# Optimization experiments

Measured on AMD Instinct MI355X. Metric: run time of the kernel, lower is better.

The kernel has to match this reference:

```python
import jax, jax.numpy as jnp
import numpy as np

N = 100000
E = 1600000
IN, HID, OUT, HEADS = 256, 16, 64, 8
NEG_SLOPE = 0.2


def gat_conv(x, src, dst, W, att_s, att_d, bias, heads, out_c, concat):
    n = x.shape[0]
    h = (x @ W).reshape(n, heads, out_c)              # [N,H,C]
    a_s = jnp.einsum('nhc,hc->nh', h, att_s)          # [N,H]
    a_d = jnp.einsum('nhc,hc->nh', h, att_d)          # [N,H]
    logits = jax.nn.leaky_relu(a_s[src] + a_d[dst], NEG_SLOPE)  # [E,H]
    m = jax.ops.segment_max(logits, dst, num_segments=n)        # [N,H]
    m = jnp.where(jnp.isfinite(m), m, 0.0)
    e = jnp.exp(logits - m[dst])                                 # [E,H]
    denom = jax.ops.segment_sum(e, dst, num_segments=n)         # [N,H]
    alpha = e / (denom[dst] + 1e-16)                             # [E,H]
    msg = h[src] * alpha[:, :, None]                             # [E,H,C]
    out = jax.ops.segment_sum(msg, dst, num_segments=n)          # [N,H,C]
    out = out.reshape(n, heads * out_c) if concat else out.mean(axis=1)
    return out + bias


def setup_inputs() -> dict:
    key = jax.random.key(0)
    ks = jax.random.split(key, 10)
    g = lambda k, shp, fan: jax.random.normal(k, shp, jnp.float32) * np.sqrt(2.0 / fan)
    x = jax.random.normal(ks[0], (N, IN), jnp.float32)
    edge_index = jax.random.randint(ks[1], (2, E), 0, N, jnp.int32)
    W1 = g(ks[2], (IN, HEADS * HID), IN)
    att1_s = g(ks[3], (HEADS, HID), HID)
    att1_d = g(ks[4], (HEADS, HID), HID)
    b1 = jnp.zeros((HEADS * HID,), jnp.float32)
    W2 = g(ks[5], (HEADS * HID, OUT), HEADS * HID)
    att2_s = g(ks[6], (1, OUT), OUT)
    att2_d = g(ks[7], (1, OUT), OUT)
    b2 = jnp.zeros((OUT,), jnp.float32)
    return {"x": x, "edge_index": edge_index, "W1": W1, "att1_s": att1_s,
            "att1_d": att1_d, "b1": b1, "W2": W2, "att2_s": att2_s,
            "att2_d": att2_d, "b2": b2}


def reference(x, edge_index, W1, att1_s, att1_d, b1, W2, att2_s, att2_d, b2):
    src, dst = edge_index[0], edge_index[1]
    h = gat_conv(x, src, dst, W1, att1_s, att1_d, b1, HEADS, HID, True)
    h = jax.nn.elu(h)  # dropout = identity in eval mode
    h = gat_conv(h, src, dst, W2, att2_s, att2_d, b2, 1, OUT, False)
    return jax.nn.log_softmax(h, axis=1)
```

## Files before the change

kernel.cpp:

```cpp
#include <hip/hip_runtime.h>
#include <math.h>

#define N_NODES 100000
#define N_EDGES 1600000
#define GEMM1_BLOCKS ((N_NODES + 63) / 64)
#define NBKT 196
#define PART_BLOCKS ((N_EDGES + 4095) / 4096)

typedef __attribute__((ext_vector_type(8))) short short8;
typedef __attribute__((ext_vector_type(4))) float floatx4;

__device__ __forceinline__ float lrelu(float v) {
    return (v > 0.f) ? v : 0.2f * v;
}

__device__ __forceinline__ unsigned short f2bf(float f) {
    unsigned int u = __float_as_uint(f);
    u += 0x7fff + ((u >> 16) & 1);
    return (unsigned short)(u >> 16);
}

__device__ __forceinline__ float bflo(unsigned int u) { return __uint_as_float(u << 16); }
__device__ __forceinline__ float bfhi(unsigned int u) { return __uint_as_float(u & 0xffff0000u); }
__device__ __forceinline__ float bfs(unsigned short s) { return __uint_as_float(((unsigned int)s) << 16); }

__global__ void prep_kernel(const float* __restrict__ W1, const float* __restrict__ W2,
                            unsigned short* __restrict__ w1b, unsigned short* __restrict__ w2b) {
    int idx = blockIdx.x * 256 + threadIdx.x;
    if (idx < 4096) {
        int lane = idx & 63;
        int ts = idx >> 6;
        int t = ts >> 3, ks = ts & 7;
        int quad = lane >> 4, l15 = lane & 15;
        int kbase = ks * 32 + quad * 8;
        unsigned short o[8];
        #pragma unroll
        for (int j = 0; j < 8; j++)
            o[j] = f2bf(W1[(size_t)(kbase + j) * 128 + t * 16 + l15]);
        uint4 pk;
        pk.x = o[0] | ((unsigned int)o[1] << 16);
        pk.y = o[2] | ((unsigned int)o[3] << 16);
        pk.z = o[4] | ((unsigned int)o[5] << 16);
        pk.w = o[6] | ((unsigned int)o[7] << 16);
        ((uint4*)w1b)[idx] = pk;
    } else if (idx < 4096 + 1024) {
        int idx2 = idx - 4096;
        int lane = idx2 & 63;
        int ts = idx2 >> 6;
        int t = ts >> 2, ks = ts & 3;
        int quad = lane >> 4, l15 = lane & 15;
        int kbase = ks * 32 + quad * 8;
        unsigned short o[8];
        #pragma unroll
        for (int j = 0; j < 8; j++)
            o[j] = f2bf(W2[(size_t)(kbase + j) * 64 + t * 16 + l15]);
        uint4 pk;
        pk.x = o[0] | ((unsigned int)o[1] << 16);
        pk.y = o[2] | ((unsigned int)o[3] << 16);
        pk.z = o[4] | ((unsigned int)o[5] << 16);
        pk.w = o[6] | ((unsigned int)o[7] << 16);
        ((uint4*)w2b)[idx2] = pk;
    }
}

__global__ void __launch_bounds__(256) hist_kernel(const int* __restrict__ ei,
                                                   int* __restrict__ bkt_count) {
    __shared__ int h[NBKT];
    for (int i = threadIdx.x; i < NBKT; i += 256) h[i] = 0;
    __syncthreads();
    int base = blockIdx.x * 4096;
    #pragma unroll
    for (int it = 0; it < 16; it++) {
        int e = base + it * 256 + (int)threadIdx.x;
        if (e < N_EDGES) atomicAdd(&h[ei[N_EDGES + e] >> 9], 1);
    }
    __syncthreads();
    for (int i = threadIdx.x; i < NBKT; i += 256)
        if (h[i]) atomicAdd(&bkt_count[i], h[i]);
}

__global__ void scan_kernel(const int* __restrict__ bkt_count, int* __restrict__ bkt_base,
                            int* __restrict__ bkt_cursor) {
    __shared__ int ps[256];
    int tid = threadIdx.x;
    int v = (tid < NBKT) ? bkt_count[tid] : 0;
    ps[tid] = v;
    __syncthreads();
    for (int off = 1; off < 256; off <<= 1) {
        int t = (tid >= off) ? ps[tid - off] : 0;
        __syncthreads();
        ps[tid] += t;
        __syncthreads();
    }
    int excl = (tid > 0) ? ps[tid - 1] : 0;
    if (tid < NBKT) { bkt_base[tid] = excl; bkt_cursor[tid] = excl; }
    if (tid == NBKT) bkt_base[NBKT] = N_EDGES;
}

__global__ void __launch_bounds__(256) part_kernel(const int* __restrict__ ei,
                                                   int* __restrict__ bkt_cursor,
                                                   int* __restrict__ ebuf) {
    __shared__ int lcnt[NBKT];
    __shared__ int lbase[NBKT];
    for (int i = threadIdx.x; i < NBKT; i += 256) lcnt[i] = 0;
    __syncthreads();
    int base = blockIdx.x * 4096;
    int pk[16], bb[16];
    #pragma unroll
    for (int it = 0; it < 16; it++) {
        int e = base + it * 256 + (int)threadIdx.x;
        bb[it] = -1;
        pk[it] = 0;
        if (e < N_EDGES) {
            int s = ei[e];
            int d = ei[N_EDGES + e];
            bb[it] = d >> 9;
            pk[it] = s | ((d & 511) << 17);
            atomicAdd(&lcnt[bb[it]], 1);
        }
    }
    __syncthreads();
    for (int i = threadIdx.x; i < NBKT; i += 256) {
        int c = lcnt[i];
        lbase[i] = c ? atomicAdd(&bkt_cursor[i], c) : 0;
        lcnt[i] = 0;
    }
    __syncthreads();
    #pragma unroll
    for (int it = 0; it < 16; it++) {
        if (bb[it] >= 0) {
            int off = atomicAdd(&lcnt[bb[it]], 1);
            ebuf[lbase[bb[it]] + off] = pk[it];
        }
    }
}

__global__ void __launch_bounds__(256) csr2_kernel(const int* __restrict__ ebuf,
                                                   const int* __restrict__ bkt_base,
                                                   int* __restrict__ rowstart,
                                                   int* __restrict__ deg,
                                                   int* __restrict__ csr_src) {
    __shared__ int h[512];
    __shared__ int cur[512];
    __shared__ int ps[256];
    const int b = blockIdx.x;
    const int s = bkt_base[b];
    const int e = bkt_base[b + 1];
    const int tid = threadIdx.x;
    h[tid] = 0;
    h[tid + 256] = 0;
    __syncthreads();
    for (int i = s + tid; i < e; i += 256)
        atomicAdd(&h[((unsigned)ebuf[i]) >> 17], 1);
    __syncthreads();
    int a0 = h[2 * tid], a1 = h[2 * tid + 1];
    ps[tid] = a0 + a1;
    __syncthreads();
    for (int off = 1; off < 256; off <<= 1) {
        int t = (tid >= off) ? ps[tid - off] : 0;
        __syncthreads();
        ps[tid] += t;
        __syncthreads();
    }
    int pbase = (tid > 0) ? ps[tid - 1] : 0;
    int n0 = b * 512 + 2 * tid;
    int n1 = n0 + 1;
    cur[2 * tid] = s + pbase;
    cur[2 * tid + 1] = s + pbase + a0;
    if (n0 < N_NODES) { rowstart[n0] = s + pbase; deg[n0] = a0; }
    if (n1 < N_NODES) { rowstart[n1] = s + pbase + a0; deg[n1] = a1; }
    __syncthreads();
    for (int i = s + tid; i < e; i += 256) {
        unsigned pkv = (unsigned)ebuf[i];
        int pos = atomicAdd(&cur[pkv >> 17], 1);
        csr_src[pos] = pkv & 0x1FFFF;
    }
}

__global__ void __launch_bounds__(256) gemm1_kernel(
        const float* __restrict__ x, const short8* __restrict__ w1b,
        const float* __restrict__ att_s, const float* __restrict__ att_d,
        unsigned short* __restrict__ h1b, float* __restrict__ a1s, float* __restrict__ a1d) {
    const int gid = blockIdx.x;
    const int lane = threadIdx.x & 63;
    const int wv = threadIdx.x >> 6;
    const int quad = lane >> 4;
    const int l15 = lane & 15;
    const int M = N_NODES;

    const int rowA = gid * 64 + wv * 16 + l15;
    const bool rowAok = rowA < M;
    const float4* xrow4 = (const float4*)(x + (size_t)rowA * 256);

    floatx4 acc[8];
    #pragma unroll
    for (int t = 0; t < 8; t++) acc[t] = (floatx4){0.f, 0.f, 0.f, 0.f};

    #pragma unroll
    for (int ks = 0; ks < 8; ks++) {
        float4 p0, p1;
        if (rowAok) {
            p0 = xrow4[ks * 8 + quad * 2];
            p1 = xrow4[ks * 8 + quad * 2 + 1];
        } else {
            p0 = make_float4(0.f, 0.f, 0.f, 0.f);
            p1 = p0;
        }
        short8 af;
        af[0] = (short)f2bf(p0.x); af[1] = (short)f2bf(p0.y);
        af[2] = (short)f2bf(p0.z); af[3] = (short)f2bf(p0.w);
        af[4] = (short)f2bf(p1.x); af[5] = (short)f2bf(p1.y);
        af[6] = (short)f2bf(p1.z); af[7] = (short)f2bf(p1.w);
        #pragma unroll
        for (int t = 0; t < 8; t++) {
            short8 bf = w1b[(t * 8 + ks) * 64 + lane];
            acc[t] = __builtin_amdgcn_mfma_f32_16x16x32_bf16(af, bf, acc[t], 0, 0, 0);
        }
    }

    const int rowC0 = gid * 64 + wv * 16 + quad * 4;
    #pragma unroll
    for (int t = 0; t < 8; t++) {
        float asw = att_s[t * 16 + l15];
        float adw = att_d[t * 16 + l15];
        #pragma unroll
        for (int r = 0; r < 4; r++) {
            int grow = rowC0 + r;
            float c = acc[t][r];
            if (grow < M) h1b[(size_t)grow * 128 + t * 16 + l15] = f2bf(c);
            float ps = c * asw;
            float pd = c * adw;
            ps += __shfl_xor(ps, 1, 64); ps += __shfl_xor(ps, 2, 64);
            ps += __shfl_xor(ps, 4, 64); ps += __shfl_xor(ps, 8, 64);
            pd += __shfl_xor(pd, 1, 64); pd += __shfl_xor(pd, 2, 64);
            pd += __shfl_xor(pd, 4, 64); pd += __shfl_xor(pd, 8, 64);
            if (l15 == 0 && grow < M) { a1s[grow * 8 + t] = ps; a1d[grow * 8 + t] = pd; }
        }
    }
}

__global__ void __launch_bounds__(256) agg1_kernel(
        const unsigned short* __restrict__ h1b, const float* __restrict__ a1s,
        const float* __restrict__ a1d, const int* __restrict__ rowstart,
        const int* __restrict__ deg, const int* __restrict__ csr_src,
        const float* __restrict__ b1, unsigned int* __restrict__ h2b, int n) {
    const int lane = threadIdx.x & 63;
    const int node = blockIdx.x * 4 + (threadIdx.x >> 6);
    if (node >= n) return;
    const int h = lane >> 3;
    const int start = rowstart[node];
    const int d = deg[node];
    const float ad = a1d[node * 8 + h];
    float l = 0.f, acc0 = 0.f, acc1 = 0.f;
    int i = 0;
    for (; i + 8 <= d; i += 8) {
        int s[8];
        float as[8];
        unsigned int u[8];
        #pragma unroll
        for (int k = 0; k < 8; k++) s[k] = csr_src[start + i + k];
        #pragma unroll
        for (int k = 0; k < 8; k++) as[k] = a1s[s[k] * 8 + h];
        #pragma unroll
        for (int k = 0; k < 8; k++)
            u[k] = *(const unsigned int*)(h1b + (size_t)s[k] * 128 + lane * 2);
        #pragma unroll
        for (int k = 0; k < 8; k++) {
            float e = __expf(lrelu(as[k] + ad));
            l += e;
            acc0 += e * bflo(u[k]);
            acc1 += e * bfhi(u[k]);
        }
    }
    for (; i + 4 <= d; i += 4) {
        int s[4];
        float as[4];
        unsigned int u[4];
        #pragma unroll
        for (int k = 0; k < 4; k++) s[k] = csr_src[start + i + k];
        #pragma unroll
        for (int k = 0; k < 4; k++) as[k] = a1s[s[k] * 8 + h];
        #pragma unroll
        for (int k = 0; k < 4; k++)
            u[k] = *(const unsigned int*)(h1b + (size_t)s[k] * 128 + lane * 2);
        #pragma unroll
        for (int k = 0; k < 4; k++) {
            float e = __expf(lrelu(as[k] + ad));
            l += e;
            acc0 += e * bflo(u[k]);
            acc1 += e * bfhi(u[k]);
        }
    }
    for (; i < d; i++) {
        int s0 = csr_src[start + i];
        float as0 = a1s[s0 * 8 + h];
        unsigned int u0 = *(const unsigned int*)(h1b + (size_t)s0 * 128 + lane * 2);
        float e0 = __expf(lrelu(as0 + ad));
        l += e0;
        acc0 += e0 * bflo(u0);
        acc1 += e0 * bfhi(u0);
    }
    float inv = 1.f / (l + 1e-16f);
    float v0 = acc0 * inv + b1[lane * 2];
    float v1 = acc1 * inv + b1[lane * 2 + 1];
    v0 = (v0 > 0.f) ? v0 : expm1f(v0);
    v1 = (v1 > 0.f) ? v1 : expm1f(v1);
    h2b[(size_t)node * 64 + lane] = (unsigned int)f2bf(v0) | ((unsigned int)f2bf(v1) << 16);
}

__global__ void __launch_bounds__(256) gemm2_kernel(
        const short8* __restrict__ h2f, const short8* __restrict__ w2b,
        const float* __restrict__ att_s, const float* __restrict__ att_d,
        unsigned short* __restrict__ t2b, float* __restrict__ a2s, float* __restrict__ a2d,
        int n) {
    const int lane = threadIdx.x & 63;
    const int wv = threadIdx.x >> 6;
    const int quad = lane >> 4;
    const int l15 = lane & 15;

    const int rowA = blockIdx.x * 64 + wv * 16 + l15;
    const bool rowAok = rowA < n;

    floatx4 acc[4];
    #pragma unroll
    for (int t = 0; t < 4; t++) acc[t] = (floatx4){0.f, 0.f, 0.f, 0.f};

    #pragma unroll
    for (int ks = 0; ks < 4; ks++) {
        short8 af = {0, 0, 0, 0, 0, 0, 0, 0};
        if (rowAok) af = h2f[(size_t)rowA * 16 + ks * 4 + quad];
        #pragma unroll
        for (int t = 0; t < 4; t++) {
            short8 bf = w2b[(t * 4 + ks) * 64 + lane];
            acc[t] = __builtin_amdgcn_mfma_f32_16x16x32_bf16(af, bf, acc[t], 0, 0, 0);
        }
    }

    const int rowC0 = blockIdx.x * 64 + wv * 16 + quad * 4;
    float asw[4], adw[4];
    #pragma unroll
    for (int t = 0; t < 4; t++) {
        asw[t] = att_s[t * 16 + l15];
        adw[t] = att_d[t * 16 + l15];
    }
    #pragma unroll
    for (int r = 0; r < 4; r++) {
        int grow = rowC0 + r;
        bool ok = grow < n;
        float ps = 0.f, pd = 0.f;
        #pragma unroll
        for (int t = 0; t < 4; t++) {
            float c = acc[t][r];
            if (ok) t2b[(size_t)grow * 64 + t * 16 + l15] = f2bf(c);
            ps += c * asw[t];
            pd += c * adw[t];
        }
        ps += __shfl_xor(ps, 1, 64); ps += __shfl_xor(ps, 2, 64);
        ps += __shfl_xor(ps, 4, 64); ps += __shfl_xor(ps, 8, 64);
        pd += __shfl_xor(pd, 1, 64); pd += __shfl_xor(pd, 2, 64);
        pd += __shfl_xor(pd, 4, 64); pd += __shfl_xor(pd, 8, 64);
        if (l15 == 0 && ok) { a2s[grow] = ps; a2d[grow] = pd; }
    }
}

__global__ void __launch_bounds__(256) agg2_kernel(
        const unsigned short* __restrict__ t2b, const float* __restrict__ a2s,
        const float* __restrict__ a2d, const int* __restrict__ rowstart,
        const int* __restrict__ deg, const int* __restrict__ csr_src,
        const float* __restrict__ b2, float* __restrict__ out, int n) {
    const int lane = threadIdx.x & 63;
    const int node = blockIdx.x * 4 + (threadIdx.x >> 6);
    if (node >= n) return;
    const int start = rowstart[node];
    const int d = deg[node];
    const float ad = a2d[node];
    float l = 0.f, acc = 0.f;
    int i = 0;
    for (; i + 8 <= d; i += 8) {
        int s[8];
        float as[8];
        unsigned short u[8];
        #pragma unroll
        for (int k = 0; k < 8; k++) s[k] = csr_src[start + i + k];
        #pragma unroll
        for (int k = 0; k < 8; k++) as[k] = a2s[s[k]];
        #pragma unroll
        for (int k = 0; k < 8; k++) u[k] = t2b[(size_t)s[k] * 64 + lane];
        #pragma unroll
        for (int k = 0; k < 8; k++) {
            float e = __expf(lrelu(as[k] + ad));
            l += e;
            acc += e * bfs(u[k]);
        }
    }
    for (; i + 4 <= d; i += 4) {
        int s[4];
        float as[4];
        unsigned short u[4];
        #pragma unroll
        for (int k = 0; k < 4; k++) s[k] = csr_src[start + i + k];
        #pragma unroll
        for (int k = 0; k < 4; k++) as[k] = a2s[s[k]];
        #pragma unroll
        for (int k = 0; k < 4; k++) u[k] = t2b[(size_t)s[k] * 64 + lane];
        #pragma unroll
        for (int k = 0; k < 4; k++) {
            float e = __expf(lrelu(as[k] + ad));
            l += e;
            acc += e * bfs(u[k]);
        }
    }
    for (; i < d; i++) {
        int s0 = csr_src[start + i];
        float as0 = a2s[s0];
        unsigned short u0 = t2b[(size_t)s0 * 64 + lane];
        float e0 = __expf(lrelu(as0 + ad));
        l += e0;
        acc += e0 * bfs(u0);
    }
    float v = acc / (l + 1e-16f) + b2[lane];
    float mx = v;
    #pragma unroll
    for (int off = 32; off >= 1; off >>= 1) mx = fmaxf(mx, __shfl_xor(mx, off, 64));
    float ex = expf(v - mx);
    float s2 = ex;
    #pragma unroll
    for (int off = 32; off >= 1; off >>= 1) s2 += __shfl_xor(s2, off, 64);
    out[(size_t)node * 64 + lane] = v - mx - logf(s2);
}


extern "C" void kernel_launch(void* const* d_in, const int* in_sizes, int n_in,
                              void* d_out, int out_size, void* d_ws, size_t ws_size,
                              hipStream_t stream) {
    const float* x     = (const float*)d_in[0];
    const int*   ei    = (const int*)d_in[1];
    const float* W1    = (const float*)d_in[2];
    const float* att1s = (const float*)d_in[3];
    const float* att1d = (const float*)d_in[4];
    const float* b1    = (const float*)d_in[5];
    const float* W2    = (const float*)d_in[6];
    const float* att2s = (const float*)d_in[7];
    const float* att2d = (const float*)d_in[8];
    const float* b2    = (const float*)d_in[9];
    float* out = (float*)d_out;

    const int N = N_NODES, E = N_EDGES;

    char* p = (char*)d_ws;
    auto take = [&](size_t bytes) {
        char* r = p;
        p += (bytes + 255) & ~(size_t)255;
        return (void*)r;
    };
    int*            bkt_count  = (int*)take(256 * 4);
    int*            bkt_base   = (int*)take(257 * 4);
    int*            bkt_cursor = (int*)take(256 * 4);
    int*            ebuf       = (int*)take((size_t)E * 4);
    int*            deg        = (int*)take((size_t)N * 4);
    int*            rowstart   = (int*)take((size_t)N * 4);
    int*            csr_src    = (int*)take((size_t)E * 4);
    unsigned short* w1b        = (unsigned short*)take(64 * 64 * 16);
    unsigned short* w2b        = (unsigned short*)take(16 * 64 * 16);
    unsigned short* h1b        = (unsigned short*)take((size_t)N * 128 * 2);
    float*          a1s        = (float*)take((size_t)N * 8 * 4);
    float*          a1d        = (float*)take((size_t)N * 8 * 4);
    unsigned int*   h2b        = (unsigned int*)take((size_t)N * 64 * 4);
    unsigned short* t2b        = (unsigned short*)take((size_t)N * 64 * 2);
    float* a2s = a1s;
    float* a2d = a1d;

    hipMemsetAsync(bkt_count, 0, 256 * 4, stream);

    prep_kernel<<<20, 256, 0, stream>>>(W1, W2, w1b, w2b);
    hist_kernel<<<PART_BLOCKS, 256, 0, stream>>>(ei, bkt_count);
    scan_kernel<<<1, 256, 0, stream>>>(bkt_count, bkt_base, bkt_cursor);
    part_kernel<<<PART_BLOCKS, 256, 0, stream>>>(ei, bkt_cursor, ebuf);
    csr2_kernel<<<NBKT, 256, 0, stream>>>(ebuf, bkt_base, rowstart, deg, csr_src);
    gemm1_kernel<<<GEMM1_BLOCKS, 256, 0, stream>>>(
        x, (const short8*)w1b, att1s, att1d, h1b, a1s, a1d);
    agg1_kernel<<<(N + 3) / 4, 256, 0, stream>>>(h1b, a1s, a1d, rowstart, deg, csr_src,
                                                 b1, h2b, N);
    gemm2_kernel<<<(N + 63) / 64, 256, 0, stream>>>((const short8*)h2b, (const short8*)w2b,
                                                    att2s, att2d, t2b, a2s, a2d, N);
    agg2_kernel<<<(N + 3) / 4, 256, 0, stream>>>(t2b, a2s, a2d, rowstart, deg, csr_src,
                                                 b2, out, N);
}
```

Baseline: 428.5 us.

## Split GEMM1 blocks across CSR-build kernels to overlap with graph preprocessing

Removes the standalone GEMM1 launch and spreads its row blocks across the hist, part and csr2 kernels as extra trailing blocks. The aim is to fill idle compute units during the small, latency-bound CSR construction kernels, and to cut one launch. The risk is that GEMM blocks compete for bandwidth with the partition work, and that the fixed split ratios may not balance well.

```diff
diff --git a/kernel.cpp b/kernel.cpp
--- a/kernel.cpp
+++ b/kernel.cpp
@@ -6,6 +6,9 @@
 #define GEMM1_BLOCKS ((N_NODES + 63) / 64)
 #define NBKT 196
 #define PART_BLOCKS ((N_EDGES + 4095) / 4096)
+#define GEMM_K1 400
+#define GEMM_K3 700
+#define GEMM_K4 (GEMM1_BLOCKS - GEMM_K1 - GEMM_K3)
 
 typedef __attribute__((ext_vector_type(8))) short short8;
 typedef __attribute__((ext_vector_type(4))) float floatx4;
@@ -23,6 +26,67 @@
 __device__ __forceinline__ float bflo(unsigned int u) { return __uint_as_float(u << 16); }
 __device__ __forceinline__ float bfhi(unsigned int u) { return __uint_as_float(u & 0xffff0000u); }
 __device__ __forceinline__ float bfs(unsigned short s) { return __uint_as_float(((unsigned int)s) << 16); }
+
+__device__ __forceinline__ void gemm1_body(
+        int gid, const float* __restrict__ x, const short8* __restrict__ w1b,
+        const float* __restrict__ att_s, const float* __restrict__ att_d,
+        unsigned short* __restrict__ h1b, float* __restrict__ a1s, float* __restrict__ a1d) {
+    const int lane = threadIdx.x & 63;
+    const int wv = threadIdx.x >> 6;
+    const int quad = lane >> 4;
+    const int l15 = lane & 15;
+    const int M = N_NODES;
+
+    const int rowA = gid * 64 + wv * 16 + l15;
+    const bool rowAok = rowA < M;
+    const float4* xrow4 = (const float4*)(x + (size_t)rowA * 256);
+
+    floatx4 acc[8];
+    #pragma unroll
+    for (int t = 0; t < 8; t++) acc[t] = (floatx4){0.f, 0.f, 0.f, 0.f};
+
+    #pragma unroll
+    for (int ks = 0; ks < 8; ks++) {
+        float4 p0, p1;
+        if (rowAok) {
+            p0 = xrow4[ks * 8 + quad * 2];
+            p1 = xrow4[ks * 8 + quad * 2 + 1];
+        } else {
+            p0 = make_float4(0.f, 0.f, 0.f, 0.f);
+            p1 = p0;
+        }
+        short8 af;
+        af[0] = (short)f2bf(p0.x); af[1] = (short)f2bf(p0.y);
+        af[2] = (short)f2bf(p0.z); af[3] = (short)f2bf(p0.w);
+        af[4] = (short)f2bf(p1.x); af[5] = (short)f2bf(p1.y);
+        af[6] = (short)f2bf(p1.z); af[7] = (short)f2bf(p1.w);
+        #pragma unroll
+        for (int t = 0; t < 8; t++) {
+            short8 bf = w1b[(t * 8 + ks) * 64 + lane];
+            acc[t] = __builtin_amdgcn_mfma_f32_16x16x32_bf16(af, bf, acc[t], 0, 0, 0);
+        }
+    }
+
+    const int rowC0 = gid * 64 + wv * 16 + quad * 4;
+    #pragma unroll
+    for (int t = 0; t < 8; t++) {
+        float asw = att_s[t * 16 + l15];
+        float adw = att_d[t * 16 + l15];
+        #pragma unroll
+        for (int r = 0; r < 4; r++) {
+            int grow = rowC0 + r;
+            float c = acc[t][r];
+            if (grow < M) h1b[(size_t)grow * 128 + t * 16 + l15] = f2bf(c);
+            float ps = c * asw;
+            float pd = c * adw;
+            ps += __shfl_xor(ps, 1, 64); ps += __shfl_xor(ps, 2, 64);
+            ps += __shfl_xor(ps, 4, 64); ps += __shfl_xor(ps, 8, 64);
+            pd += __shfl_xor(pd, 1, 64); pd += __shfl_xor(pd, 2, 64);
+            pd += __shfl_xor(pd, 4, 64); pd += __shfl_xor(pd, 8, 64);
+            if (l15 == 0 && grow < M) { a1s[grow * 8 + t] = ps; a1d[grow * 8 + t] = pd; }
+        }
+    }
+}
 
 __global__ void prep_kernel(const float* __restrict__ W1, const float* __restrict__ W2,
                             unsigned short* __restrict__ w1b, unsigned short* __restrict__ w2b) {
@@ -63,12 +127,20 @@
     }
 }
 
-__global__ void __launch_bounds__(256) hist_kernel(const int* __restrict__ ei,
-                                                   int* __restrict__ bkt_count) {
+__global__ void __launch_bounds__(256) hist_gemm_kernel(
+        const int* __restrict__ ei, int* __restrict__ bkt_count,
+        const float* __restrict__ x, const short8* __restrict__ w1b,
+        const float* __restrict__ att_s, const float* __restrict__ att_d,
+        unsigned short* __restrict__ h1b, float* __restrict__ a1s, float* __restrict__ a1d) {
+    const int bid = blockIdx.x;
+    if (bid >= PART_BLOCKS) {
+        gemm1_body(bid - PART_BLOCKS, x, w1b, att_s, att_d, h1b, a1s, a1d);
+        return;
+    }
     __shared__ int h[NBKT];
     for (int i = threadIdx.x; i < NBKT; i += 256) h[i] = 0;
     __syncthreads();
-    int base = blockIdx.x * 4096;
+    int base = bid * 4096;
     #pragma unroll
     for (int it = 0; it < 16; it++) {
         int e = base + it * 256 + (int)threadIdx.x;
@@ -97,14 +169,21 @@
     if (tid == NBKT) bkt_base[NBKT] = N_EDGES;
 }
 
-__global__ void __launch_bounds__(256) part_kernel(const int* __restrict__ ei,
-                                                   int* __restrict__ bkt_cursor,
-                                                   int* __restrict__ ebuf) {
+__global__ void __launch_bounds__(256) part_gemm_kernel(
+        const int* __restrict__ ei, int* __restrict__ bkt_cursor, int* __restrict__ ebuf,
+        const float* __restrict__ x, const short8* __restrict__ w1b,
+        const float* __restrict__ att_s, const float* __restrict__ att_d,
+        unsigned short* __restrict__ h1b, float* __restrict__ a1s, float* __restrict__ a1d) {
+    const int bid = blockIdx.x;
+    if (bid >= PART_BLOCKS) {
+        gemm1_body(bid - PART_BLOCKS + GEMM_K1, x, w1b, att_s, att_d, h1b, a1s, a1d);
+        return;
+    }
     __shared__ int lcnt[NBKT];
     __shared__ int lbase[NBKT];
     for (int i = threadIdx.x; i < NBKT; i += 256) lcnt[i] = 0;
     __syncthreads();
-    int base = blockIdx.x * 4096;
+    int base = bid * 4096;
     int pk[16], bb[16];
     #pragma unroll
     for (int it = 0; it < 16; it++) {
@@ -135,15 +214,21 @@
     }
 }
 
-__global__ void __launch_bounds__(256) csr2_kernel(const int* __restrict__ ebuf,
-                                                   const int* __restrict__ bkt_base,
-                                                   int* __restrict__ rowstart,
-                                                   int* __restrict__ deg,
-                                                   int* __restrict__ csr_src) {
+__global__ void __launch_bounds__(256) csr2_gemm_kernel(
+        const int* __restrict__ ebuf, const int* __restrict__ bkt_base,
+        int* __restrict__ rowstart, int* __restrict__ deg, int* __restrict__ csr_src,
+        const float* __restrict__ x, const short8* __restrict__ w1b,
+        const float* __restrict__ att_s, const float* __restrict__ att_d,
+        unsigned short* __restrict__ h1b, float* __restrict__ a1s, float* __restrict__ a1d) {
+    const int bid = blockIdx.x;
+    if (bid >= NBKT) {
+        gemm1_body(bid - NBKT + GEMM_K1 + GEMM_K3, x, w1b, att_s, att_d, h1b, a1s, a1d);
+        return;
+    }
     __shared__ int h[512];
     __shared__ int cur[512];
     __shared__ int ps[256];
-    const int b = blockIdx.x;
+    const int b = bid;
     const int s = bkt_base[b];
     const int e = bkt_base[b + 1];
     const int tid = threadIdx.x;
@@ -174,68 +259,6 @@
         unsigned pkv = (unsigned)ebuf[i];
         int pos = atomicAdd(&cur[pkv >> 17], 1);
         csr_src[pos] = pkv & 0x1FFFF;
-    }
-}
-
-__global__ void __launch_bounds__(256) gemm1_kernel(
-        const float* __restrict__ x, const short8* __restrict__ w1b,
-        const float* __restrict__ att_s, const float* __restrict__ att_d,
-        unsigned short* __restrict__ h1b, float* __restrict__ a1s, float* __restrict__ a1d) {
-    const int gid = blockIdx.x;
-    const int lane = threadIdx.x & 63;
-    const int wv = threadIdx.x >> 6;
-    const int quad = lane >> 4;
-    const int l15 = lane & 15;
-    const int M = N_NODES;
-
-    const int rowA = gid * 64 + wv * 16 + l15;
-    const bool rowAok = rowA < M;
-    const float4* xrow4 = (const float4*)(x + (size_t)rowA * 256);
-
-    floatx4 acc[8];
-    #pragma unroll
-    for (int t = 0; t < 8; t++) acc[t] = (floatx4){0.f, 0.f, 0.f, 0.f};
-
-    #pragma unroll
-    for (int ks = 0; ks < 8; ks++) {
-        float4 p0, p1;
-        if (rowAok) {
-            p0 = xrow4[ks * 8 + quad * 2];
-            p1 = xrow4[ks * 8 + quad * 2 + 1];
-        } else {
-            p0 = make_float4(0.f, 0.f, 0.f, 0.f);
-            p1 = p0;
-        }
-        short8 af;
-        af[0] = (short)f2bf(p0.x); af[1] = (short)f2bf(p0.y);
-        af[2] = (short)f2bf(p0.z); af[3] = (short)f2bf(p0.w);
-        af[4] = (short)f2bf(p1.x); af[5] = (short)f2bf(p1.y);
-        af[6] = (short)f2bf(p1.z); af[7] = (short)f2bf(p1.w);
-        #pragma unroll
-        for (int t = 0; t < 8; t++) {
-            short8 bf = w1b[(t * 8 + ks) * 64 + lane];
-            acc[t] = __builtin_amdgcn_mfma_f32_16x16x32_bf16(af, bf, acc[t], 0, 0, 0);
-        }
-    }
-
-    const int rowC0 = gid * 64 + wv * 16 + quad * 4;
-    #pragma unroll
-    for (int t = 0; t < 8; t++) {
-        float asw = att_s[t * 16 + l15];
-        float adw = att_d[t * 16 + l15];
-        #pragma unroll
-        for (int r = 0; r < 4; r++) {
-            int grow = rowC0 + r;
-            float c = acc[t][r];
-            if (grow < M) h1b[(size_t)grow * 128 + t * 16 + l15] = f2bf(c);
-            float ps = c * asw;
-            float pd = c * adw;
-            ps += __shfl_xor(ps, 1, 64); ps += __shfl_xor(ps, 2, 64);
-            ps += __shfl_xor(ps, 4, 64); ps += __shfl_xor(ps, 8, 64);
-            pd += __shfl_xor(pd, 1, 64); pd += __shfl_xor(pd, 2, 64);
-            pd += __shfl_xor(pd, 4, 64); pd += __shfl_xor(pd, 8, 64);
-            if (l15 == 0 && grow < M) { a1s[grow * 8 + t] = ps; a1d[grow * 8 + t] = pd; }
-        }
     }
 }
 
@@ -473,11 +496,13 @@
     hipMemsetAsync(bkt_count, 0, 256 * 4, stream);
 
     prep_kernel<<<20, 256, 0, stream>>>(W1, W2, w1b, w2b);
-    hist_kernel<<<PART_BLOCKS, 256, 0, stream>>>(ei, bkt_count);
+    hist_gemm_kernel<<<PART_BLOCKS + GEMM_K1, 256, 0, stream>>>(
+        ei, bkt_count, x, (const short8*)w1b, att1s, att1d, h1b, a1s, a1d);
     scan_kernel<<<1, 256, 0, stream>>>(bkt_count, bkt_base, bkt_cursor);
-    part_kernel<<<PART_BLOCKS, 256, 0, stream>>>(ei, bkt_cursor, ebuf);
-    csr2_kernel<<<NBKT, 256, 0, stream>>>(ebuf, bkt_base, rowstart, deg, csr_src);
-    gemm1_kernel<<<GEMM1_BLOCKS, 256, 0, stream>>>(
+    part_gemm_kernel<<<PART_BLOCKS + GEMM_K3, 256, 0, stream>>>(
+        ei, bkt_cursor, ebuf, x, (const short8*)w1b, att1s, att1d, h1b, a1s, a1d);
+    csr2_gemm_kernel<<<NBKT + GEMM_K4, 256, 0, stream>>>(
+        ebuf, bkt_base, rowstart, deg, csr_src,
         x, (const short8*)w1b, att1s, att1d, h1b, a1s, a1d);
     agg1_kernel<<<(N + 3) / 4, 256, 0, stream>>>(h1b, a1s, a1d, rowstart, deg, csr_src,
                                                  b1, h2b, N);
```

New measurement: 417.2 us. -2.7%, faster.
